# Optimization experiments

Measured on AMD Instinct MI355X. Metric: run time of the kernel, lower is better.

Reference implementation:

```python
import jax, jax.numpy as jnp
import numpy as np

NUM_SPECIAL = 3  # rows 1..NUM_SPECIAL in special table; row 0 is padding (zeros)

def setup_inputs() -> dict:
    key = jax.random.key(0)
    ks = jax.random.split(key, 16)
    T, B, E, H, L, V = 128, 32, 512, 512, 2, 32000
    G = 4 * H
    s = 0.02
    special_emb = jax.random.normal(ks[1], (NUM_SPECIAL + 1, E), jnp.float32) * s
    special_emb = special_emb.at[0].set(0.0)  # padding_idx=0
    return {
        "ids": jax.random.randint(ks[0], (T, B), 0, V),
        "length_countdown": jax.random.uniform(ks[2], (T, B, 1), jnp.float32),
        "word_emb": jax.random.normal(ks[3], (V, E), jnp.float32) * s,
        "special_emb": special_emb,
        "h0": jax.random.normal(ks[4], (L, B, H), jnp.float32) * s,
        "c0": jax.random.normal(ks[5], (L, B, H), jnp.float32) * s,
        "prev_output": jnp.zeros((B, H), jnp.float32),
        "Wih0": jax.random.normal(ks[6], (G, E + H + 1), jnp.float32) * s,
        "Whh0": jax.random.normal(ks[7], (G, H), jnp.float32) * s,
        "bih0": jnp.zeros((G,), jnp.float32),
        "bhh0": jnp.zeros((G,), jnp.float32),
        "Wih1": jax.random.normal(ks[8], (G, H), jnp.float32) * s,
        "Whh1": jax.random.normal(ks[9], (G, H), jnp.float32) * s,
        "bih1": jnp.zeros((G,), jnp.float32),
        "bhh1": jnp.zeros((G,), jnp.float32),
        "Wg": jax.random.normal(ks[10], (V, H), jnp.float32) * s,
        "bg": jnp.zeros((V,), jnp.float32),
    }

def _lstm_cell(x, h, c, Wih, Whh, bih, bhh):
    gates = x @ Wih.T + bih + h @ Whh.T + bhh  # [B, 4H]
    i, f, g, o = jnp.split(gates, 4, axis=-1)  # torch LSTMCell gate order
    c_new = jax.nn.sigmoid(f) * c + jax.nn.sigmoid(i) * jnp.tanh(g)
    h_new = jax.nn.sigmoid(o) * jnp.tanh(c_new)
    return h_new, c_new

def reference(ids, length_countdown, word_emb, special_emb, h0, c0, prev_output,
              Wih0, Whh0, bih0, bhh0, Wih1, Whh1, bih1, bhh1, Wg, bg):
    # embeddings = word_embeddings(ids) + special_embeddings(special_ids(ids))
    sp_ids = jnp.where(ids < NUM_SPECIAL, ids + 1, 0)
    emb = word_emb[ids] + special_emb[sp_ids]                 # [T,B,E]
    rnn_in = jnp.concatenate([emb, length_countdown], axis=2)  # [T,B,E+1]

    Wihs = (Wih0, Wih1); Whhs = (Whh0, Whh1)
    bihs = (bih0, bih1); bhhs = (bhh0, bhh1)
    L = h0.shape[0]

    def step(carry, emb_t):
        out, h, c = carry
        x = jnp.concatenate([emb_t, out], axis=1)  # input feeding
        hs, cs = [], []
        for l in range(L):
            h_l, c_l = _lstm_cell(x, h[l], c[l], Wihs[l], Whhs[l], bihs[l], bhhs[l])
            x = h_l  # dropout=0
            hs.append(h_l); cs.append(c_l)
        out = x
        score = jax.nn.log_softmax(out @ Wg.T + bg, axis=-1)  # generator
        return (out, jnp.stack(hs), jnp.stack(cs)), score

    (out, hT, cT), scores = jax.lax.scan(step, (prev_output, h0, c0), rnn_in)
    return scores, (hT, cT), out
```

## Files before the change

### kernel.cpp

```cpp
#include <hip/hip_runtime.h>
#include <hip/hip_bf16.h>


typedef __attribute__((ext_vector_type(8))) short bf16x8;
typedef __attribute__((ext_vector_type(4))) float f32x4;
typedef __attribute__((ext_vector_type(2))) unsigned long long u64x2;

#define AS1 __attribute__((address_space(1)))
#define AS3 __attribute__((address_space(3)))
#define RLX __ATOMIC_RELAXED
#define AGT __HIP_MEMORY_SCOPE_AGENT
#define NGEN 176
#define NSUB 48

__device__ __forceinline__ unsigned short f2bf(float f) {
  unsigned int u = __builtin_bit_cast(unsigned int, f);
  u += 0x7fffu + ((u >> 16) & 1u);
  return (unsigned short)(u >> 16);
}

__device__ __forceinline__ void gl16(const void* g, void* l) {
  __builtin_amdgcn_global_load_lds((const AS1 unsigned int*)g,
                                   (AS3 unsigned int*)l, 16, 0, 0);
}

__device__ __forceinline__ float sigm(float x) { return 1.0f / (1.0f + __expf(-x)); }

__global__ __launch_bounds__(256, 1) void prep_k(
    const float* __restrict__ Wg,  const float* __restrict__ Wih0,
    const float* __restrict__ Whh0,const float* __restrict__ Wih1,
    const float* __restrict__ Whh1,const float* __restrict__ bih0,
    const float* __restrict__ bhh0,const float* __restrict__ bih1,
    const float* __restrict__ bhh1,const float* __restrict__ h0,
    const float* __restrict__ pout,
    unsigned short* __restrict__ WgBf, unsigned short* __restrict__ W0e,
    unsigned short* __restrict__ Wr0p, unsigned short* __restrict__ Wr1p,
    float* __restrict__ b1p, float* __restrict__ bias0c,
    float* __restrict__ wcd, unsigned short* __restrict__ H0X,
    unsigned short* __restrict__ FOUT, unsigned short* __restrict__ H1I)
{
  const long N0 = 16384000L;
  const long N1 = N0 + 1048576L;
  const long N2 = N1 + 2097152L;
  const long N3 = N2 + 2097152L;
  const long N4 = N3 + 2048L;
  const long N5 = N4 + 2048L;
  const long N6 = N5 + 2048L;
  const long N7 = N6 + 49152L;
  for (long i = blockIdx.x * 256L + threadIdx.x; i < N7; i += 256L * gridDim.x) {
    if (i < N0) {
      WgBf[i] = f2bf(Wg[i]);
    } else if (i < N1) {
      long k = i - N0; int g = (int)(k >> 9); int kk = (int)(k & 511);
      W0e[k] = f2bf(Wih0[g * 1025 + kk]);
    } else if (i < N2) {
      long k = i - N1; int gp = (int)(k >> 10); int kk = (int)(k & 1023);
      int j = gp >> 2, gate = gp & 3; int g = gate * 512 + j;
      float v = (kk < 512) ? Whh0[g * 512 + kk] : Wih0[g * 1025 + 513 + (kk - 512)];
      Wr0p[k] = f2bf(v);
    } else if (i < N3) {
      long k = i - N2; int gp = (int)(k >> 10); int kk = (int)(k & 1023);
      int j = gp >> 2, gate = gp & 3; int g = gate * 512 + j;
      float v = (kk < 512) ? Wih1[g * 512 + kk] : Whh1[g * 512 + (kk - 512)];
      Wr1p[k] = f2bf(v);
    } else if (i < N4) {
      int gp = (int)(i - N3); int j = gp >> 2, gate = gp & 3; int g = gate * 512 + j;
      b1p[gp] = bih1[g] + bhh1[g];
    } else if (i < N5) {
      int g = (int)(i - N4); bias0c[g] = bih0[g] + bhh0[g];
    } else if (i < N6) {
      int g = (int)(i - N5); wcd[g] = Wih0[g * 1025 + 512];
    } else {
      long k = i - N6;
      int sub = (int)(k >> 14);
      int e = (int)(k & 16383);
      int wgx = e >> 9, b = (e >> 4) & 31, jl = e & 15;
      int j = wgx * 16 + jl;
      float v = (sub == 0) ? h0[b * 512 + j]
              : (sub == 1) ? h0[16384 + b * 512 + j]
                           : pout[b * 512 + j];
      unsigned short* dst = (sub == 0) ? H0X : (sub == 1) ? H1I : FOUT;
      dst[e] = f2bf(v);
    }
  }
}

__global__ __launch_bounds__(256, 1) void emb_k(
    const int* __restrict__ ids, const float* __restrict__ wemb,
    const float* __restrict__ semb, unsigned short* __restrict__ ebf)
{
  const int tb = blockIdx.x;
  const int id = ids[tb];
  const int sp = (id < 3) ? (id + 1) : 0;
  const float* wr = wemb + (long)id * 512;
  const float* sr = semb + sp * 512;
  for (int i = threadIdx.x; i < 512; i += 256)
    ebf[tb * 512 + i] = f2bf(wr[i] + sr[i]);
}

__global__ __launch_bounds__(256, 1) void gemm_p0(
    const unsigned short* __restrict__ A,
    const unsigned short* __restrict__ B, int N,
    float* __restrict__ C,
    const float* __restrict__ e0, const float* __restrict__ e1,
    const float* __restrict__ e2)
{
  __shared__ unsigned short sA[4096];
  __shared__ unsigned short sB[4096];
  const int tid = threadIdx.x;
  const int l = tid & 63, w = tid >> 6;
  const int nb = N >> 7;
  const int bid = blockIdx.x;
  const int bm = bid / nb, bn = bid - bm * nb;

  const int u0 = w * 128 + l;
  const int u1 = u0 + 64;
  const int r0 = u0 >> 2, c0 = (u0 & 3) ^ (r0 & 3);
  const int r1 = u1 >> 2, c1 = (u1 & 3) ^ (r1 & 3);
  const unsigned short* ga0 = A + (long)(bm * 128 + r0) * 512 + c0 * 8;
  const unsigned short* ga1 = A + (long)(bm * 128 + r1) * 512 + c1 * 8;
  const unsigned short* gb0 = B + (long)(bn * 128 + r0) * 512 + c0 * 8;
  const unsigned short* gb1 = B + (long)(bn * 128 + r1) * 512 + c1 * 8;
  unsigned short* la0 = sA + (w * 2 + 0) * 512;
  unsigned short* la1 = sA + (w * 2 + 1) * 512;
  unsigned short* lb0 = sB + (w * 2 + 0) * 512;
  unsigned short* lb1 = sB + (w * 2 + 1) * 512;

  const int fr = l & 15, fc = l >> 4;
  const int wm = w >> 1, wn = w & 1;
  int aoff[4], boff[4];
#pragma unroll
  for (int mi = 0; mi < 4; ++mi) {
    int row = wm * 64 + mi * 16 + fr;
    aoff[mi] = row * 64 + ((fc ^ (row & 3)) * 16);
  }
#pragma unroll
  for (int ni = 0; ni < 4; ++ni) {
    int row = wn * 64 + ni * 16 + fr;
    boff[ni] = row * 64 + ((fc ^ (row & 3)) * 16);
  }

  f32x4 acc[4][4];
#pragma unroll
  for (int i = 0; i < 4; ++i)
#pragma unroll
    for (int jq = 0; jq < 4; ++jq) acc[i][jq] = (f32x4){0.f, 0.f, 0.f, 0.f};

  for (int kt = 0; kt < 16; ++kt) {
    __syncthreads();
    gl16(ga0 + kt * 32, la0);
    gl16(ga1 + kt * 32, la1);
    gl16(gb0 + kt * 32, lb0);
    gl16(gb1 + kt * 32, lb1);
    asm volatile("s_waitcnt vmcnt(0)" ::: "memory");
    __syncthreads();
    bf16x8 av[4], bv[4];
#pragma unroll
    for (int mi = 0; mi < 4; ++mi)
      av[mi] = *(const bf16x8*)((const char*)sA + aoff[mi]);
#pragma unroll
    for (int ni = 0; ni < 4; ++ni)
      bv[ni] = *(const bf16x8*)((const char*)sB + boff[ni]);
#pragma unroll
    for (int mi = 0; mi < 4; ++mi)
#pragma unroll
      for (int ni = 0; ni < 4; ++ni)
        acc[mi][ni] = __builtin_amdgcn_mfma_f32_16x16x32_bf16(av[mi], bv[ni], acc[mi][ni], 0, 0, 0);
  }

  const int mbase = bm * 128 + wm * 64;
  const int nbase = bn * 128 + wn * 64;
#pragma unroll
  for (int mi = 0; mi < 4; ++mi)
#pragma unroll
    for (int ni = 0; ni < 4; ++ni) {
      const int col = nbase + ni * 16 + fr;
#pragma unroll
      for (int r = 0; r < 4; ++r) {
        const int row = mbase + mi * 16 + fc * 4 + r;
        const int gp = ((row & 511) << 2) | (row >> 9);
        float v = acc[mi][ni][r] + e0[row] + e2[col] * e1[row];
        C[(long)gp * N + col] = v;
      }
    }
}

__global__ __launch_bounds__(256, 1) void lstm_seq(
    const unsigned short* __restrict__ Wr0p,
    const unsigned short* __restrict__ Wr1p,
    float* __restrict__ P0t, const float* __restrict__ b1p,
    const float* __restrict__ c0in,
    unsigned short* __restrict__ H0X, unsigned short* __restrict__ H1X,
    const unsigned short* __restrict__ FOUT, const unsigned short* __restrict__ H1I,
    unsigned short* __restrict__ outbf, float* __restrict__ outs,
    unsigned int* __restrict__ flagA, unsigned int* __restrict__ flagB,
    unsigned int* __restrict__ flagC, unsigned int* __restrict__ cntBM,
    const unsigned short* __restrict__ WgBf, const float* __restrict__ bg)
{
  const int tid = threadIdx.x;
  __shared__ char smem[75264] __attribute__((aligned(16)));

  if (blockIdx.x < 32) {
    unsigned short* sx = (unsigned short*)smem;
    float (*sg)[65] = (float(*)[65])(smem + 65536);
    unsigned short (*sh)[16] = (unsigned short(*)[16])(smem + 73856);

    const int wg = blockIdx.x;
    const int l = tid & 63, w = tid >> 6;
    const int fr = l & 15, fc = l >> 4;
    const int b = tid & 31, jl0 = tid >> 5;
    const int sb = l >> 1, sjh = l & 1;

    float c0r[2], c1r[2], h0k[2], h1k[2];
#pragma unroll
    for (int jq = 0; jq < 2; ++jq) {
      c0r[jq] = c0in[b * 512 + wg * 16 + jl0 + jq * 8];
      c1r[jq] = c0in[16384 + b * 512 + wg * 16 + jl0 + jq * 8];
      h0k[jq] = 0.f; h1k[jq] = 0.f;
    }

    float b1v[8];
#pragma unroll
    for (int jq = 0; jq < 2; ++jq)
#pragma unroll
      for (int g = 0; g < 4; ++g)
        b1v[jq * 4 + g] = b1p[(wg * 16 + jl0 + jq * 8) * 4 + g];

    const char* sxb0 = (const char*)sx + fr * 2048;
    const char* sxb1 = (const char*)sx + (16 + fr) * 2048;
    const int xr = (fr & 7) << 4;
    const int wrow = (wg * 64 + w * 16 + fr) * 1024 + fc * 8;

    char* const sxw = (char*)sx + sb * 2048;
    const int sswz = (sb & 7) << 4;

#define STAGE2(srcp, half)                                                    \
  do {                                                                        \
    unsigned long long q0[8], q1[8];                                          \
    _Pragma("unroll")                                                         \
    for (int i = 0; i < 8; ++i) {                                             \
      int u = i * 256 + tid;                                                  \
      q0[i] = __hip_atomic_load((const unsigned long long*)(srcp) + u * 2,    \
                                RLX, AGT);                                    \
      q1[i] = __hip_atomic_load((const unsigned long long*)(srcp) + u * 2 + 1,\
                                RLX, AGT);                                    \
    }                                                                         \
    _Pragma("unroll")                                                         \
    for (int i = 0; i < 8; ++i) {                                             \
      int cb = (half) * 1024 + (i * 4 + w) * 32 + sjh * 16;                   \
      u64x2 v; v.x = q0[i]; v.y = q1[i];                                      \
      *(u64x2*)(sxw + (cb ^ sswz)) = v;                                       \
    }                                                                         \
  } while (0)

#define MFMA_HALF(Wp, k0, a0v, a1v)                                           \
  do {                                                                        \
    _Pragma("unroll")                                                         \
    for (int kt = (k0); kt < (k0) + 16; ++kt) {                               \
      bf16x8 bv = *(const bf16x8*)((Wp) + wrow + kt * 32);                    \
      bf16x8 x0 = *(const bf16x8*)(sxb0 + ((kt * 64 + fc * 16) ^ xr));        \
      bf16x8 x1 = *(const bf16x8*)(sxb1 + ((kt * 64 + fc * 16) ^ xr));        \
      a0v = __builtin_amdgcn_mfma_f32_16x16x32_bf16(x0, bv, a0v, 0, 0, 0);    \
      a1v = __builtin_amdgcn_mfma_f32_16x16x32_bf16(x1, bv, a1v, 0, 0, 0);    \
    }                                                                         \
  } while (0)

#define POLL(flags, tgt)                                                      \
  do {                                                                        \
    const unsigned int* fp = (flags) + ((l & 31) << 5);                       \
    for (;;) {                                                                \
      unsigned int f = __hip_atomic_load(fp, RLX, AGT);                       \
      if (__all((int)(f >= (unsigned int)(tgt)))) break;                      \
      __builtin_amdgcn_s_sleep(1);                                            \
    }                                                                         \
    asm volatile("" ::: "memory");                                            \
  } while (0)

    STAGE2(H0X, 0);
    __syncthreads();
    if (tid == 0)
      __hip_atomic_store(&flagB[wg << 5], 1u, RLX, AGT);

    for (int t = 0; t < 128; ++t) {
      float p0v[8];
#pragma unroll
      for (int jq = 0; jq < 2; ++jq)
#pragma unroll
        for (int g = 0; g < 4; ++g)
          p0v[jq * 4 + g] =
              P0t[(long)((wg * 16 + jl0 + jq * 8) * 4 + g) * 4096 + t * 32 + b];

      f32x4 accA0 = (f32x4){0.f, 0.f, 0.f, 0.f};
      f32x4 accA1 = (f32x4){0.f, 0.f, 0.f, 0.f};
      MFMA_HALF(Wr0p, 0, accA0, accA1);

      POLL(flagB, t + 1);
      if (t == 0) STAGE2(FOUT, 1); else STAGE2(H1X, 1);
      __syncthreads();
      MFMA_HALF(Wr0p, 16, accA0, accA1);
#pragma unroll
      for (int r = 0; r < 4; ++r) {
        sg[fc * 4 + r][w * 16 + fr] = accA0[r];
        sg[16 + fc * 4 + r][w * 16 + fr] = accA1[r];
      }
      __syncthreads();
#pragma unroll
      for (int jq = 0; jq < 2; ++jq) {
        const int jl = jl0 + jq * 8;
        float gi = sg[b][jl * 4 + 0] + p0v[jq * 4 + 0];
        float gf = sg[b][jl * 4 + 1] + p0v[jq * 4 + 1];
        float gg = sg[b][jl * 4 + 2] + p0v[jq * 4 + 2];
        float go = sg[b][jl * 4 + 3] + p0v[jq * 4 + 3];
        float cn = sigm(gf) * c0r[jq] + sigm(gi) * tanhf(gg);
        float hn = sigm(go) * tanhf(cn);
        c0r[jq] = cn; h0k[jq] = hn;
        sh[b][jl] = f2bf(hn);
      }
      __syncthreads();
      if (w == 0) {
        u64x2 v = *(const u64x2*)&sh[sb][sjh * 8];
        unsigned long long* dst =
            (unsigned long long*)(H0X + wg * 512 + sb * 16 + sjh * 8);
        __hip_atomic_store(dst,     v.x, RLX, AGT);
        __hip_atomic_store(dst + 1, v.y, RLX, AGT);
        asm volatile("s_waitcnt vmcnt(0)" ::: "memory");
        if (tid == 0)
          __hip_atomic_store(&flagA[wg << 5], (unsigned int)(t + 1), RLX, AGT);
      }

      f32x4 accB0 = (f32x4){0.f, 0.f, 0.f, 0.f};
      f32x4 accB1 = (f32x4){0.f, 0.f, 0.f, 0.f};
      if (t == 0) {
        STAGE2(H1I, 1);
        __syncthreads();
      }
      MFMA_HALF(Wr1p, 16, accB0, accB1);

      POLL(flagA, t + 1);
      STAGE2(H0X, 0);
      __syncthreads();
      MFMA_HALF(Wr1p, 0, accB0, accB1);
#pragma unroll
      for (int r = 0; r < 4; ++r) {
        sg[fc * 4 + r][w * 16 + fr] = accB0[r];
        sg[16 + fc * 4 + r][w * 16 + fr] = accB1[r];
      }
      __syncthreads();
#pragma unroll
      for (int jq = 0; jq < 2; ++jq) {
        const int jl = jl0 + jq * 8;
        float gi = sg[b][jl * 4 + 0] + b1v[jq * 4 + 0];
        float gf = sg[b][jl * 4 + 1] + b1v[jq * 4 + 1];
        float gg = sg[b][jl * 4 + 2] + b1v[jq * 4 + 2];
        float go = sg[b][jl * 4 + 3] + b1v[jq * 4 + 3];
        float cn = sigm(gf) * c1r[jq] + sigm(gi) * tanhf(gg);
        float hn = sigm(go) * tanhf(cn);
        c1r[jq] = cn; h1k[jq] = hn;
        sh[b][jl] = f2bf(hn);
      }
      __syncthreads();
      if (w == 0) {
        u64x2 v = *(const u64x2*)&sh[sb][sjh * 8];
        unsigned long long* dst =
            (unsigned long long*)(H1X + wg * 512 + sb * 16 + sjh * 8);
        __hip_atomic_store(dst,     v.x, RLX, AGT);
        __hip_atomic_store(dst + 1, v.y, RLX, AGT);
        asm volatile("s_waitcnt vmcnt(0)" ::: "memory");
        if (tid == 0)
          __hip_atomic_store(&flagB[wg << 5], (unsigned int)(t + 2), RLX, AGT);
      } else if (w == 1) {
        const unsigned long long* s = (const unsigned long long*)&sh[sb][sjh * 8];
        unsigned long long* dst =
            (unsigned long long*)(outbf + (t * 32 + sb) * 512 + wg * 16 + sjh * 8);
        __hip_atomic_store(dst,     s[0], RLX, AGT);
        __hip_atomic_store(dst + 1, s[1], RLX, AGT);
        asm volatile("s_waitcnt vmcnt(0)" ::: "memory");
        if (l == 0)
          __hip_atomic_store(&flagC[wg << 5], (unsigned int)(t + 1), RLX, AGT);
      }
    }
#undef STAGE2
#undef MFMA_HALF
#undef POLL

    float* hT = outs + 131072000;
    float* cT = outs + 131072000 + 32768;
    float* oT = outs + 131072000 + 65536;
#pragma unroll
    for (int jq = 0; jq < 2; ++jq) {
      const int j = wg * 16 + jl0 + jq * 8;
      hT[b * 512 + j] = h0k[jq];
      hT[16384 + b * 512 + j] = h1k[jq];
      cT[b * 512 + j] = c0r[jq];
      cT[16384 + b * 512 + j] = c1r[jq];
      oT[b * 512 + j] = h1k[jq];
    }
    return;
  }

  if (blockIdx.x < 32 + NGEN) {
    unsigned short* sA = (unsigned short*)smem;
    unsigned short* sB = (unsigned short*)(smem + 8192);
    float (*pmw)[2][2] = (float(*)[2][2])(smem + 16384);

    const int g = (int)blockIdx.x - 32;
    const int l = tid & 63, w = tid >> 6;
    const int fr = l & 15, fc = l >> 4;
    const int wm = w >> 1, wn = w & 1;

    const int u0 = w * 128 + l, u1 = u0 + 64;
    const int r0 = u0 >> 2, c0 = (u0 & 3) ^ (r0 & 3);
    const int r1 = u1 >> 2, c1 = (u1 & 3) ^ (r1 & 3);
    unsigned short* lb0 = sB + (w * 2 + 0) * 512;
    unsigned short* lb1 = sB + (w * 2 + 1) * 512;

    int aoff[4], boff[4];
#pragma unroll
    for (int mi = 0; mi < 4; ++mi) {
      int row = wm * 64 + mi * 16 + fr;
      aoff[mi] = row * 64 + ((fc ^ (row & 3)) * 16);
    }
#pragma unroll
    for (int ni = 0; ni < 4; ++ni) {
      int row = wn * 64 + ni * 16 + fr;
      boff[ni] = row * 64 + ((fc ^ (row & 3)) * 16);
    }

    for (int job = g; job < 8000; job += NGEN) {
      const int bm = job / 250, bn = job - bm * 250;

      if (w == 0) {
        const unsigned int* fp = flagC + ((l & 31) << 5);
        const unsigned int tgt = (unsigned int)(4 * bm + 4);
        for (;;) {
          unsigned int f = __hip_atomic_load(fp, RLX, AGT);
          if (__all((int)(f >= tgt))) break;
          __builtin_amdgcn_s_sleep(16);
        }
        asm volatile("" ::: "memory");
      }
      __syncthreads();

      const unsigned short* Ab0 = outbf + (long)(bm * 128 + r0) * 512 + c0 * 8;
      const unsigned short* Ab1 = outbf + (long)(bm * 128 + r1) * 512 + c1 * 8;
      const unsigned short* gb0 = WgBf + (long)(bn * 128 + r0) * 512 + c0 * 8;
      const unsigned short* gb1 = WgBf + (long)(bn * 128 + r1) * 512 + c1 * 8;

      f32x4 acc[4][4];
#pragma unroll
      for (int i = 0; i < 4; ++i)
#pragma unroll
        for (int jq = 0; jq < 4; ++jq) acc[i][jq] = (f32x4){0.f, 0.f, 0.f, 0.f};

      for (int kt = 0; kt < 16; ++kt) {
        __syncthreads();
        unsigned long long a0x = __hip_atomic_load((const unsigned long long*)(Ab0 + kt * 32),     RLX, AGT);
        unsigned long long a0y = __hip_atomic_load((const unsigned long long*)(Ab0 + kt * 32) + 1, RLX, AGT);
        unsigned long long a1x = __hip_atomic_load((const unsigned long long*)(Ab1 + kt * 32),     RLX, AGT);
        unsigned long long a1y = __hip_atomic_load((const unsigned long long*)(Ab1 + kt * 32) + 1, RLX, AGT);
        gl16(gb0 + kt * 32, lb0);
        gl16(gb1 + kt * 32, lb1);
        { u64x2 va; va.x = a0x; va.y = a0y; *(u64x2*)((char*)sA + u0 * 16) = va; }
        { u64x2 va; va.x = a1x; va.y = a1y; *(u64x2*)((char*)sA + u1 * 16) = va; }
        asm volatile("s_waitcnt vmcnt(0)" ::: "memory");
        __syncthreads();
        bf16x8 av[4], bv[4];
#pragma unroll
        for (int mi = 0; mi < 4; ++mi)
          av[mi] = *(const bf16x8*)((const char*)sA + aoff[mi]);
#pragma unroll
        for (int ni = 0; ni < 4; ++ni)
          bv[ni] = *(const bf16x8*)((const char*)sB + boff[ni]);
#pragma unroll
        for (int mi = 0; mi < 4; ++mi)
#pragma unroll
          for (int ni = 0; ni < 4; ++ni)
            acc[mi][ni] = __builtin_amdgcn_mfma_f32_16x16x32_bf16(av[mi], bv[ni], acc[mi][ni], 0, 0, 0);
      }

      const int mbase = bm * 128 + wm * 64;
      const int nbase = bn * 128 + wn * 64;
      float m2[4][4], s2[4][4];
#pragma unroll
      for (int mi = 0; mi < 4; ++mi)
#pragma unroll
        for (int r = 0; r < 4; ++r) { m2[mi][r] = -3.0e38f; s2[mi][r] = 0.f; }
#pragma unroll
      for (int mi = 0; mi < 4; ++mi)
#pragma unroll
        for (int ni = 0; ni < 4; ++ni) {
          const int col = nbase + ni * 16 + fr;
          const float bgc = bg[col];
#pragma unroll
          for (int r = 0; r < 4; ++r) {
            float v = acc[mi][ni][r] + bgc;
            acc[mi][ni][r] = v;
            __hip_atomic_store(&outs[(long)(mbase + mi * 16 + fc * 4 + r) * 32000L + col],
                               v, RLX, AGT);
            m2[mi][r] = fmaxf(m2[mi][r], v);
          }
        }
#pragma unroll
      for (int mi = 0; mi < 4; ++mi)
#pragma unroll
        for (int r = 0; r < 4; ++r)
#pragma unroll
          for (int s = 1; s < 16; s <<= 1)
            m2[mi][r] = fmaxf(m2[mi][r], __shfl_xor(m2[mi][r], s));
#pragma unroll
      for (int mi = 0; mi < 4; ++mi)
#pragma unroll
        for (int ni = 0; ni < 4; ++ni)
#pragma unroll
          for (int r = 0; r < 4; ++r)
            s2[mi][r] += __expf(acc[mi][ni][r] - m2[mi][r]);
#pragma unroll
      for (int mi = 0; mi < 4; ++mi)
#pragma unroll
        for (int r = 0; r < 4; ++r)
#pragma unroll
          for (int s = 1; s < 16; s <<= 1)
            s2[mi][r] += __shfl_xor(s2[mi][r], s);
      if (fr == 0) {
#pragma unroll
        for (int mi = 0; mi < 4; ++mi)
#pragma unroll
          for (int r = 0; r < 4; ++r) {
            const int rl = wm * 64 + mi * 16 + fc * 4 + r;
            pmw[rl][wn][0] = m2[mi][r];
            pmw[rl][wn][1] = s2[mi][r];
          }
      }
      __syncthreads();
      if (tid < 128) {
        float ma = pmw[tid][0][0], sa = pmw[tid][0][1];
        float mb = pmw[tid][1][0], sb2 = pmw[tid][1][1];
        float M = fmaxf(ma, mb);
        float S = sa * __expf(ma - M) + sb2 * __expf(mb - M);
        int q2 = 2 * (tid * 250 + bn);
        unsigned long long* p = (unsigned long long*)
            (P0t + ((long)(q2 >> 7)) * 4096 + 128L * bm + (q2 & 127));
        float2 o; o.x = M; o.y = S;
        __hip_atomic_store(p, __builtin_bit_cast(unsigned long long, o), RLX, AGT);
      }
      asm volatile("s_waitcnt vmcnt(0)" ::: "memory");
      __syncthreads();
      if (tid == 0)
        __hip_atomic_fetch_add(&cntBM[bm << 5], 1u, RLX, AGT);
      __syncthreads();
    }
    return;
  }

  {
    float* red = (float*)smem;
    const int s = (int)blockIdx.x - 32 - NGEN;

    for (int row = s; row < 4096; row += NSUB) {
      const int bm = row >> 7, rl = row & 127;
      if (tid == 0) {
        for (;;) {
          unsigned c = __hip_atomic_load(&cntBM[bm << 5], RLX, AGT);
          if (c >= 250u) break;
          __builtin_amdgcn_s_sleep(32);
        }
      }
      __syncthreads();
      asm volatile("" ::: "memory");

      float m = -3.0e38f, sm = 0.0f;
      if (tid < 250) {
        int q2 = 2 * (rl * 250 + tid);
        const unsigned long long* pp = (const unsigned long long*)
            (P0t + ((long)(q2 >> 7)) * 4096 + 128L * bm + (q2 & 127));
        unsigned long long q = __hip_atomic_load(pp, RLX, AGT);
        float2 f = __builtin_bit_cast(float2, q);
        m = f.x; sm = f.y;
      }
#pragma unroll
      for (int off = 32; off > 0; off >>= 1) {
        float mo = __shfl_down(m, off);
        float so = __shfl_down(sm, off);
        float mn = fmaxf(m, mo);
        sm = sm * __expf(m - mn) + so * __expf(mo - mn);
        m = mn;
      }
      if ((tid & 63) == 0) { red[tid >> 6] = m; red[4 + (tid >> 6)] = sm; }
      __syncthreads();
      if (tid == 0) {
        float M = red[0], S = red[4];
#pragma unroll
        for (int i = 1; i < 4; ++i) {
          float mn = fmaxf(M, red[i]);
          S = S * __expf(M - mn) + red[4 + i] * __expf(red[i] - mn);
          M = mn;
        }
        red[8] = M + __logf(S);
      }
      __syncthreads();
      const float lse = red[8];

      float* pr = outs + (long)row * 32000L;
#pragma unroll 2
      for (int i = tid; i < 8000; i += 256) {
        const unsigned long long* lp = (const unsigned long long*)(pr + i * 4);
        unsigned long long qa = __hip_atomic_load(lp,     RLX, AGT);
        unsigned long long qb = __hip_atomic_load(lp + 1, RLX, AGT);
        float2 fa = __builtin_bit_cast(float2, qa);
        float2 fb = __builtin_bit_cast(float2, qb);
        float4 v;
        v.x = fa.x - lse; v.y = fa.y - lse; v.z = fb.x - lse; v.w = fb.y - lse;
        *(float4*)(pr + i * 4) = v;
      }
      __syncthreads();
    }
  }
}

extern "C" void kernel_launch(void* const* d_in, const int* in_sizes, int n_in,
                              void* d_out, int out_size, void* d_ws, size_t ws_size,
                              hipStream_t stream) {
  const int*   ids  = (const int*)d_in[0];
  const float* cd   = (const float*)d_in[1];
  const float* wemb = (const float*)d_in[2];
  const float* semb = (const float*)d_in[3];
  const float* h0   = (const float*)d_in[4];
  const float* c0   = (const float*)d_in[5];
  const float* pout = (const float*)d_in[6];
  const float* Wih0 = (const float*)d_in[7];
  const float* Whh0 = (const float*)d_in[8];
  const float* bih0 = (const float*)d_in[9];
  const float* bhh0 = (const float*)d_in[10];
  const float* Wih1 = (const float*)d_in[11];
  const float* Whh1 = (const float*)d_in[12];
  const float* bih1 = (const float*)d_in[13];
  const float* bhh1 = (const float*)d_in[14];
  const float* Wg   = (const float*)d_in[15];
  const float* bg   = (const float*)d_in[16];
  float* out = (float*)d_out;

  char* ws = (char*)d_ws;
  unsigned short* WgBf   = (unsigned short*)(ws);
  unsigned short* W0e    = (unsigned short*)(ws + 32768000);
  unsigned short* Wr0p   = (unsigned short*)(ws + 34865152);
  unsigned short* Wr1p   = (unsigned short*)(ws + 39059456);
  float*          b1p    = (float*)(ws + 43253760);
  float*          bias0c = (float*)(ws + 43261952);
  float*          wcd    = (float*)(ws + 43270144);
  unsigned short* embbf  = (unsigned short*)(ws + 43278336);
  unsigned short* outbf  = (unsigned short*)(ws + 47472640);
  float*          P0t    = (float*)(ws + 51666944);
  unsigned int*   flagA  = (unsigned int*)(ws + 85221376);
  unsigned int*   flagB  = (unsigned int*)(ws + 85225472);
  unsigned short* H0X    = (unsigned short*)(ws + 85229568);
  unsigned short* H1X    = (unsigned short*)(ws + 85262336);
  unsigned short* FOUT   = (unsigned short*)(ws + 85295104);
  unsigned short* H1I    = (unsigned short*)(ws + 85327872);
  unsigned int*   flagC  = (unsigned int*)(ws + 85360640);
  unsigned int*   cntBM  = (unsigned int*)(ws + 85364736);

  hipMemsetAsync((void*)flagA, 0, 8192, stream);
  hipMemsetAsync((void*)flagC, 0, 8192, stream);

  prep_k<<<8192, 256, 0, stream>>>(Wg, Wih0, Whh0, Wih1, Whh1,
                                   bih0, bhh0, bih1, bhh1, h0, pout,
                                   WgBf, W0e, Wr0p, Wr1p, b1p, bias0c, wcd,
                                   H0X, FOUT, H1I);

  emb_k<<<4096, 256, 0, stream>>>(ids, wemb, semb, embbf);

  gemm_p0<<<512, 256, 0, stream>>>(W0e, embbf, 4096, P0t, bias0c, wcd, cd);

  lstm_seq<<<32 + NGEN + NSUB, 256, 0, stream>>>(Wr0p, Wr1p, P0t, b1p, c0,
                                                 H0X, H1X, FOUT, H1I, outbf, out,
                                                 flagA, flagB, flagC, cntBM,
                                                 WgBf, bg);
}
```

Before: 1.731 ms.

## Use atomic row ticket for dynamic log-softmax fixup and batch output loads

```diff
diff --git a/kernel.cpp b/kernel.cpp
--- a/kernel.cpp
+++ b/kernel.cpp
@@ -195,6 +195,7 @@
     unsigned short* __restrict__ outbf, float* __restrict__ outs,
     unsigned int* __restrict__ flagA, unsigned int* __restrict__ flagB,
     unsigned int* __restrict__ flagC, unsigned int* __restrict__ cntBM,
+    unsigned int* __restrict__ rowTk,
     const unsigned short* __restrict__ WgBf, const float* __restrict__ bg)
 {
   const int tid = threadIdx.x;
@@ -549,15 +550,20 @@
         __hip_atomic_fetch_add(&cntBM[bm << 5], 1u, RLX, AGT);
       __syncthreads();
     }
-    return;
   }
 
   {
     float* red = (float*)smem;
-    const int s = (int)blockIdx.x - 32 - NGEN;
-
-    for (int row = s; row < 4096; row += NSUB) {
-      const int bm = row >> 7, rl = row & 127;
+    unsigned* rowsh = (unsigned*)(smem + 64);
+
+    for (;;) {
+      if (tid == 0)
+        rowsh[0] = __hip_atomic_fetch_add(rowTk, 1u, RLX, AGT);
+      __syncthreads();
+      const unsigned row = rowsh[0];
+      if (row >= 4096u) break;
+      const int bm = (int)(row >> 7), rl = (int)(row & 127);
+
       if (tid == 0) {
         for (;;) {
           unsigned c = __hip_atomic_load(&cntBM[bm << 5], RLX, AGT);
@@ -601,8 +607,33 @@
       const float lse = red[8];
 
       float* pr = outs + (long)row * 32000L;
-#pragma unroll 2
-      for (int i = tid; i < 8000; i += 256) {
+#define SUBGRP(START, CNT)                                                    \
+      do {                                                                    \
+        unsigned long long qa[CNT], qb[CNT];                                  \
+        _Pragma("unroll")                                                     \
+        for (int k = 0; k < CNT; ++k) {                                       \
+          const unsigned long long* lp =                                      \
+              (const unsigned long long*)(pr + ((START + k) * 256 + tid) * 4);\
+          qa[k] = __hip_atomic_load(lp,     RLX, AGT);                        \
+          qb[k] = __hip_atomic_load(lp + 1, RLX, AGT);                        \
+        }                                                                     \
+        _Pragma("unroll")                                                     \
+        for (int k = 0; k < CNT; ++k) {                                       \
+          float2 fa = __builtin_bit_cast(float2, qa[k]);                      \
+          float2 fb = __builtin_bit_cast(float2, qb[k]);                      \
+          float4 v;                                                           \
+          v.x = fa.x - lse; v.y = fa.y - lse;                                 \
+          v.z = fb.x - lse; v.w = fb.y - lse;                                 \
+          *(float4*)(pr + ((START + k) * 256 + tid) * 4) = v;                 \
+        }                                                                     \
+      } while (0)
+      SUBGRP(0, 8);
+      SUBGRP(8, 8);
+      SUBGRP(16, 8);
+      SUBGRP(24, 7);
+#undef SUBGRP
+      if (tid < 64) {
+        const int i = 31 * 256 + tid;
         const unsigned long long* lp = (const unsigned long long*)(pr + i * 4);
         unsigned long long qa = __hip_atomic_load(lp,     RLX, AGT);
         unsigned long long qb = __hip_atomic_load(lp + 1, RLX, AGT);
@@ -658,9 +689,10 @@
   unsigned short* H1I    = (unsigned short*)(ws + 85327872);
   unsigned int*   flagC  = (unsigned int*)(ws + 85360640);
   unsigned int*   cntBM  = (unsigned int*)(ws + 85364736);
+  unsigned int*   rowTk  = (unsigned int*)(ws + 85368832);
 
   hipMemsetAsync((void*)flagA, 0, 8192, stream);
-  hipMemsetAsync((void*)flagC, 0, 8192, stream);
+  hipMemsetAsync((void*)flagC, 0, 12288, stream);
 
   prep_k<<<8192, 256, 0, stream>>>(Wg, Wih0, Whh0, Wih1, Whh1,
                                    bih0, bhh0, bih1, bhh1, h0, pout,
@@ -674,5 +706,5 @@
   lstm_seq<<<32 + NGEN + NSUB, 256, 0, stream>>>(Wr0p, Wr1p, P0t, b1p, c0,
                                                  H0X, H1X, FOUT, H1I, outbf, out,
                                                  flagA, flagB, flagC, cntBM,
-                                                 WgBf, bg);
+                                                 rowTk, WgBf, bg);
 }
```

Result: slower. 1.780 ms (+2.8%).
